# Performance work log

Measured on AMD Instinct MI355X. Metric: run time of the kernel, lower is better.

## Reference

```python
import jax, jax.numpy as jnp
import numpy as np

K = 1024      # num_embeddings
D = 256       # embedding_dim
BETA = 0.25


def setup_inputs() -> dict:
    key = jax.random.key(0)
    k1, k2 = jax.random.split(key)
    z = jax.random.normal(k1, (4, D, 16, 32, 32), dtype=jnp.float32)
    # matches torch init: uniform(-1/K, 1/K)
    embedding = jax.random.uniform(k2, (K, D), dtype=jnp.float32,
                                   minval=-1.0 / K, maxval=1.0 / K)
    return {"z": z, "embedding": embedding}


def reference(z, embedding):
    # z: (B, C, Dd, H, W) with C == D
    z_perm = jnp.transpose(z, (0, 2, 3, 4, 1))          # (B, Dd, H, W, C)
    flat = z_perm.reshape(-1, D)                        # (N, D)

    dist = (jnp.sum(flat * flat, axis=1, keepdims=True)
            + jnp.sum(embedding * embedding, axis=1)
            - 2.0 * flat @ embedding.T)
    indices_flat = jnp.argmin(dist, axis=1)             # (N,)

    # one-hot @ embedding == direct gather
    z_q_flat = embedding[indices_flat]                  # (N, D)
    z_q = z_q_flat.reshape(z_perm.shape)

    commitment_loss = jnp.mean((z_perm - jax.lax.stop_gradient(z_q)) ** 2)
    vq_loss = BETA * commitment_loss

    # straight-through estimator
    z_q_st = z_perm + jax.lax.stop_gradient(z_q - z_perm)
    z_q_out = jnp.transpose(z_q_st, (0, 4, 1, 2, 3))    # back to (B, C, Dd, H, W)

    # perplexity from assignment histogram
    n = flat.shape[0]
    counts = jnp.zeros((K,), dtype=flat.dtype).at[indices_flat].add(1.0)
    avg_probs = counts / n
    perplexity = jnp.exp(-jnp.sum(avg_probs * jnp.log(avg_probs + 1e-10)))

    indices = indices_flat.reshape(z_perm.shape[:-1])   # (B, Dd, H, W)
    return z_q_out, vq_loss, indices, perplexity
```

## Files before the change

kernel.cpp:

```cpp
#include <hip/hip_runtime.h>

#define Dd 256
#define Kc 1024
#define SPATIAL 16384
#define NROWS 65536
#define NELEM 16777216
#define LOSS_OFF 16777216
#define IDX_OFF  16777217
#define PERP_OFF (16777217 + 65536)
#define MARGIN 3.5e-4f

typedef _Float16 f16x8 __attribute__((ext_vector_type(8)));
typedef _Float16 f16x2 __attribute__((ext_vector_type(2)));
typedef float f32x4 __attribute__((ext_vector_type(4)));


__global__ __launch_bounds__(256) void prep2_kernel(const float* __restrict__ emb,
                                                    _Float16* __restrict__ ef,
                                                    float* __restrict__ se) {
  const int j = blockIdx.x, c = threadIdx.x;
  float v = emb[j * Dd + c];
  ef[j * Dd + c] = (_Float16)(v * 1024.0f);
  double s = (double)v * (double)v;
  #pragma unroll
  for (int off = 32; off; off >>= 1) s += __shfl_down(s, off, 64);
  __shared__ double ws4[4];
  if ((threadIdx.x & 63) == 0) ws4[threadIdx.x >> 6] = s;
  __syncthreads();
  if (threadIdx.x == 0) se[j] = (float)(ws4[0] + ws4[1] + ws4[2] + ws4[3]);
}

__global__ __launch_bounds__(256, 2) void prefilter2_kernel(const float* __restrict__ z,
                                                            const _Float16* __restrict__ ef,
                                                            const float* __restrict__ se,
                                                            float* __restrict__ sx,
                                                            float* __restrict__ rowmin,
                                                            int* __restrict__ candcount,
                                                            int* __restrict__ cand_g) {
  __shared__ _Float16 As[32 * 272];
  __shared__ double sxp[8][32];
  __shared__ float selds[Kc];
  __shared__ int cnts[32];
  __shared__ int cands[32][8];
  __shared__ float rminw[4][32];
  __shared__ float rthr[32];

  const int tid = threadIdx.x;
  const int n0 = blockIdx.x * 32;
  const int b = n0 >> 14, s0 = n0 & 16383;
  const float* zb = z + (size_t)b * (Dd * SPATIAL) + s0;

  {
    const int r = tid & 31, cp = tid >> 5;
    double acc = 0.0;
    #pragma unroll 8
    for (int c = cp * 32; c < cp * 32 + 32; ++c) {
      const float v = zb[(size_t)c * SPATIAL + r];
      As[r * 272 + c] = (_Float16)v;
      acc += (double)v * (double)v;
    }
    sxp[cp][r] = acc;
  }
  #pragma unroll
  for (int i = 0; i < 4; ++i) selds[tid + 256 * i] = se[tid + 256 * i];
  if (tid < 32) cnts[tid] = 0;
  __syncthreads();
  if (tid < 32) {
    double s = 0.0;
    #pragma unroll
    for (int p = 0; p < 8; ++p) s += sxp[p][tid];
    sx[n0 + tid] = (float)s;
  }

  const int w = tid >> 6, lane = tid & 63, q = lane >> 4, l15 = lane & 15;
  const int colbase = w * 256;

  f16x8 Afrag[2][8];
  #pragma unroll
  for (int rt = 0; rt < 2; ++rt)
    #pragma unroll
    for (int kk = 0; kk < 8; ++kk)
      Afrag[rt][kk] = *(const f16x8*)(&As[(rt * 16 + l15) * 272 + kk * 32 + q * 8]);

  const _Float16* efb = ef + (size_t)(colbase + l15) * Dd + q * 8;

  float rmin8[8];
  #pragma unroll
  for (int i = 0; i < 8; ++i) rmin8[i] = 3.4e38f;
  f16x2 scst[16][4];

  #pragma unroll
  for (int ct = 0; ct < 16; ++ct) {
    const _Float16* bp = efb + (size_t)ct * 16 * Dd;
    f16x8 B[8];
    #pragma unroll
    for (int kk = 0; kk < 8; ++kk) B[kk] = *(const f16x8*)(bp + kk * 32);
    f32x4 a0 = {0.f, 0.f, 0.f, 0.f}, a1 = {0.f, 0.f, 0.f, 0.f};
    #pragma unroll
    for (int kk = 0; kk < 8; ++kk) {
      a0 = __builtin_amdgcn_mfma_f32_16x16x32_f16(Afrag[0][kk], B[kk], a0, 0, 0, 0);
      a1 = __builtin_amdgcn_mfma_f32_16x16x32_f16(Afrag[1][kk], B[kk], a1, 0, 0, 0);
    }
    const float sec = selds[colbase + ct * 16 + l15];
    #pragma unroll
    for (int reg = 0; reg < 4; ++reg) {
      const float sc0 = fmaf(-0.001953125f, a0[reg], sec);
      const float sc1 = fmaf(-0.001953125f, a1[reg], sec);
      rmin8[reg]     = fminf(rmin8[reg], sc0);
      rmin8[reg + 4] = fminf(rmin8[reg + 4], sc1);
      scst[ct][reg] = (f16x2){(_Float16)sc0, (_Float16)sc1};
    }
  }

  #pragma unroll
  for (int m = 1; m <= 8; m <<= 1)
    #pragma unroll
    for (int i = 0; i < 8; ++i) rmin8[i] = fminf(rmin8[i], __shfl_xor(rmin8[i], m, 64));
  if (l15 == 0) {
    #pragma unroll
    for (int reg = 0; reg < 4; ++reg) {
      rminw[w][q * 4 + reg] = rmin8[reg];
      rminw[w][16 + q * 4 + reg] = rmin8[4 + reg];
    }
  }
  __syncthreads();
  if (tid < 32) {
    const float m = fminf(fminf(rminw[0][tid], rminw[1][tid]),
                          fminf(rminw[2][tid], rminw[3][tid]));
    rowmin[n0 + tid] = m;
    rthr[tid] = m + MARGIN;
  }
  __syncthreads();

  float thr0[4], thr1[4];
  #pragma unroll
  for (int reg = 0; reg < 4; ++reg) {
    thr0[reg] = rthr[q * 4 + reg];
    thr1[reg] = rthr[16 + q * 4 + reg];
  }
  #pragma unroll
  for (int ct = 0; ct < 16; ++ct) {
    const int col = colbase + ct * 16 + l15;
    #pragma unroll
    for (int reg = 0; reg < 4; ++reg) {
      if ((float)scst[ct][reg][0] < thr0[reg]) {
        const int pos = atomicAdd(&cnts[q * 4 + reg], 1);
        if (pos < 8) cands[q * 4 + reg][pos] = col;
      }
      if ((float)scst[ct][reg][1] < thr1[reg]) {
        const int pos = atomicAdd(&cnts[16 + q * 4 + reg], 1);
        if (pos < 8) cands[16 + q * 4 + reg][pos] = col;
      }
    }
  }
  __syncthreads();
  if (tid < 32) candcount[n0 + tid] = cnts[tid];
  cand_g[(size_t)(n0 + (tid >> 3)) * 8 + (tid & 7)] = cands[tid >> 3][tid & 7];
}

__global__ __launch_bounds__(256) void resolve_easy_kernel(const int* __restrict__ candcount,
                                                           const int* __restrict__ cand_g,
                                                           const float* __restrict__ sx,
                                                           const float* __restrict__ rowmin,
                                                           float* __restrict__ out_idx_f,
                                                           int* __restrict__ idx_i,
                                                           int* __restrict__ counts,
                                                           int* __restrict__ hardcnt,
                                                           int* __restrict__ hardlist,
                                                           double* __restrict__ loss_sum) {
  const int tid = threadIdx.x;
  const int n = blockIdx.x * 256 + tid;
  const int cnt = candcount[n];
  double lp = 0.0;
  if (cnt == 1) {
    const int j = cand_g[(size_t)n * 8];
    idx_i[n] = j;
    out_idx_f[n] = (float)j;
    atomicAdd(&counts[j], 1);
    lp = (double)sx[n] + (double)rowmin[n];
  } else {
    const int pos = atomicAdd(hardcnt, 1);
    hardlist[pos] = n;
  }
  #pragma unroll
  for (int off = 32; off; off >>= 1) lp += __shfl_down(lp, off, 64);
  __shared__ double dred[4];
  if ((tid & 63) == 0) dred[tid >> 6] = lp;
  __syncthreads();
  if (tid == 0) atomicAdd(loss_sum, dred[0] + dred[1] + dred[2] + dred[3]);
}

__global__ __launch_bounds__(256) void resolve_hard_kernel(const float* __restrict__ z,
                                                           const float* __restrict__ emb,
                                                           const float* __restrict__ se,
                                                           const float* __restrict__ sx,
                                                           const int* __restrict__ candcount,
                                                           const int* __restrict__ cand_g,
                                                           const int* __restrict__ hardcnt,
                                                           const int* __restrict__ hardlist,
                                                           float* __restrict__ out_idx_f,
                                                           int* __restrict__ idx_i,
                                                           int* __restrict__ counts,
                                                           double* __restrict__ loss_sum) {
  __shared__ float xs[4][256];
  const int tid = threadIdx.x, w = tid >> 6, lane = tid & 63;
  const int hc = *hardcnt;
  const int nw = gridDim.x * 4;
  double wloss = 0.0;
  for (int i = blockIdx.x * 4 + w; i < hc; i += nw) {
    const int n = hardlist[i];
    const int b = n >> 14, s = n & 16383;
    #pragma unroll
    for (int ro = 0; ro < 4; ++ro)
      xs[w][ro * 64 + lane] =
          z[(size_t)b * (Dd * SPATIAL) + (size_t)(ro * 64 + lane) * SPATIAL + s];
    asm volatile("s_waitcnt lgkmcnt(0) vmcnt(0)" ::: "memory");
    const int cnt = candcount[n];
    const float sxn = sx[n];
    float scb = 3.4e38f;
    int jb = 0x7fffffff;
    if (cnt <= 8) {
      if (lane < cnt) {
        jb = cand_g[(size_t)n * 8 + lane];
        const float4* ep = (const float4*)(emb + (size_t)jb * Dd);
        float acc = 0.f;
        #pragma unroll 8
        for (int kk = 0; kk < 64; ++kk) {
          const float4 e4 = ep[kk];
          const float* xp = &xs[w][kk * 4];
          acc = fmaf(xp[0], e4.x, acc);
          acc = fmaf(xp[1], e4.y, acc);
          acc = fmaf(xp[2], e4.z, acc);
          acc = fmaf(xp[3], e4.w, acc);
        }
        const float t1 = sxn + se[jb];
        scb = t1 - 2.0f * acc;
      }
    } else {
      for (int jj = 0; jj < 16; ++jj) {
        const int j = lane * 16 + jj;
        const float4* ep = (const float4*)(emb + (size_t)j * Dd);
        float acc = 0.f;
        #pragma unroll 8
        for (int kk = 0; kk < 64; ++kk) {
          const float4 e4 = ep[kk];
          const float* xp = &xs[w][kk * 4];
          acc = fmaf(xp[0], e4.x, acc);
          acc = fmaf(xp[1], e4.y, acc);
          acc = fmaf(xp[2], e4.z, acc);
          acc = fmaf(xp[3], e4.w, acc);
        }
        const float t1 = sxn + se[j];
        const float sc = t1 - 2.0f * acc;
        if (sc < scb) { scb = sc; jb = j; }
      }
    }
    #pragma unroll
    for (int m = 1; m <= 32; m <<= 1) {
      const float so = __shfl_xor(scb, m, 64);
      const int jo = __shfl_xor(jb, m, 64);
      if (so < scb || (so == scb && jo < jb)) { scb = so; jb = jo; }
    }
    if (lane == 0) {
      idx_i[n] = jb;
      out_idx_f[n] = (float)jb;
      atomicAdd(&counts[jb], 1);
      wloss += (double)sxn + (double)scb;
    }
  }
  if (lane == 0) atomicAdd(loss_sum, wloss);
}

__global__ __launch_bounds__(256) void phase2c_kernel(const float* __restrict__ emb,
                                                      const int* __restrict__ idx_i,
                                                      float* __restrict__ out_zq) {
  __shared__ float els[64 * 257];
  __shared__ int sidx[64];
  const int tid = threadIdx.x;
  const int blk = blockIdx.x, b = blk >> 8, s0 = (blk & 255) << 6;
  if (tid < 64) sidx[tid] = idx_i[b * SPATIAL + s0 + tid];
  __syncthreads();
  {
    const int rr = tid >> 2, p = tid & 3;
    const float* ep = emb + (size_t)sidx[rr] * Dd + p * 64;
    float* dl = els + rr * 257 + p * 64;
    #pragma unroll
    for (int i = 0; i < 64; i += 4) {
      const float4 e4 = *(const float4*)(ep + i);
      dl[i] = e4.x; dl[i + 1] = e4.y; dl[i + 2] = e4.z; dl[i + 3] = e4.w;
    }
  }
  __syncthreads();
  const int s = tid & 63, coff = tid >> 6;
  const size_t zb = (size_t)b * (Dd * SPATIAL);
  #pragma unroll 4
  for (int c = coff; c < Dd; c += 4)
    out_zq[zb + (size_t)c * SPATIAL + s0 + s] = els[s * 257 + c];
}

__global__ __launch_bounds__(256) void finalize_kernel(const int* __restrict__ counts,
                                                       const double* __restrict__ loss_sum,
                                                       float* __restrict__ out) {
  const int tid = threadIdx.x;
  double local = 0.0;
  for (int k = tid; k < Kc; k += 256) {
    const double p = (double)counts[k] / (double)NROWS;
    local += p * log(p + 1e-10);
  }
  #pragma unroll
  for (int off = 32; off; off >>= 1) local += __shfl_down(local, off, 64);
  __shared__ double dred[4];
  if ((tid & 63) == 0) dred[tid >> 6] = local;
  __syncthreads();
  if (tid == 0) {
    const double H = dred[0] + dred[1] + dred[2] + dred[3];
    out[PERP_OFF] = (float)exp(-H);
    out[LOSS_OFF] = (float)(0.25 * loss_sum[0] / (double)NELEM);
  }
}


__global__ __launch_bounds__(256) void prep_kernel(const float* __restrict__ emb,
                                                   float* __restrict__ eT,
                                                   float* __restrict__ se) {
  const int j = blockIdx.x, c = threadIdx.x;
  float v = emb[j * Dd + c];
  eT[c * Kc + j] = v;
  double s = (double)v * (double)v;
  #pragma unroll
  for (int off = 32; off; off >>= 1) s += __shfl_down(s, off, 64);
  __shared__ double ws4[4];
  if ((threadIdx.x & 63) == 0) ws4[threadIdx.x >> 6] = s;
  __syncthreads();
  if (threadIdx.x == 0) se[j] = (float)(ws4[0] + ws4[1] + ws4[2] + ws4[3]);
}

__global__ __launch_bounds__(256) void sx_kernel(const float* __restrict__ z,
                                                 float* __restrict__ sx) {
  __shared__ double part[4][64];
  const int tid = threadIdx.x, r = tid & 63, cg = tid >> 6;
  const int blk = blockIdx.x, b = blk >> 8, s0 = (blk & 255) << 6;
  const float* zb = z + (size_t)b * (Dd * SPATIAL);
  double acc = 0.0;
  for (int c = cg * 64; c < cg * 64 + 64; ++c) {
    const float v = zb[(size_t)c * SPATIAL + s0 + r];
    acc += (double)v * (double)v;
  }
  part[cg][r] = acc;
  __syncthreads();
  if (tid < 64)
    sx[b * SPATIAL + s0 + tid] =
        (float)(part[0][tid] + part[1][tid] + part[2][tid] + part[3][tid]);
}

__global__ __launch_bounds__(256) void argmin_kernel(const float* __restrict__ z,
                                                     const float* __restrict__ eT,
                                                     const float* __restrict__ se,
                                                     const float* __restrict__ sx,
                                                     float* __restrict__ out_idx_f,
                                                     int* __restrict__ idx_i,
                                                     int* __restrict__ counts) {
  __shared__ float As[32 * 64];
  __shared__ float Bs[32 * 64];
  __shared__ float ses[Kc];
  __shared__ float sxs[64];
  __shared__ float redS1[64 * 16];
  __shared__ int   redI1[64 * 16];
  const int tid = threadIdx.x, tc = tid & 15, tr = tid >> 4;
  const int blk = blockIdx.x, b = blk >> 8, s0 = (blk & 255) << 6;
  const float* zb = z + (size_t)b * (Dd * SPATIAL);
  #pragma unroll
  for (int i = 0; i < 4; ++i) ses[tid + 256 * i] = se[tid + 256 * i];
  if (tid < 64) sxs[tid] = sx[b * SPATIAL + s0 + tid];
  float s1[4]; int j1[4];
  #pragma unroll
  for (int r = 0; r < 4; ++r) { s1[r] = 3.4e38f; j1[r] = 0; }
  for (int j0 = 0; j0 < Kc; j0 += 64) {
    float acc[4][4];
    #pragma unroll
    for (int rr = 0; rr < 4; ++rr)
      #pragma unroll
      for (int cc = 0; cc < 4; ++cc) acc[rr][cc] = 0.0f;
    for (int c0 = 0; c0 < Dd; c0 += 32) {
      __syncthreads();
      #pragma unroll
      for (int i = 0; i < 8; ++i) {
        const int e = i * 256 + tid, ci = e >> 6, r = e & 63;
        As[e] = zb[(size_t)(c0 + ci) * SPATIAL + s0 + r];
        Bs[e] = eT[(c0 + ci) * Kc + j0 + r];
      }
      __syncthreads();
      #pragma unroll
      for (int d = 0; d < 32; ++d) {
        const float4 av = *reinterpret_cast<const float4*>(&As[d * 64 + 4 * tr]);
        const float4 bv = *reinterpret_cast<const float4*>(&Bs[d * 64 + 4 * tc]);
        const float aa[4] = {av.x, av.y, av.z, av.w};
        const float bb[4] = {bv.x, bv.y, bv.z, bv.w};
        #pragma unroll
        for (int rr = 0; rr < 4; ++rr)
          #pragma unroll
          for (int cc = 0; cc < 4; ++cc)
            acc[rr][cc] = fmaf(aa[rr], bb[cc], acc[rr][cc]);
      }
    }
    #pragma unroll
    for (int rr = 0; rr < 4; ++rr) {
      const float sxr = sxs[4 * tr + rr];
      #pragma unroll
      for (int cc = 0; cc < 4; ++cc) {
        const int j = j0 + 4 * tc + cc;
        const float t1 = sxr + ses[j];
        const float s = t1 - 2.0f * acc[rr][cc];
        if (s < s1[rr] || (s == s1[rr] && j < j1[rr])) { s1[rr] = s; j1[rr] = j; }
      }
    }
  }
  #pragma unroll
  for (int rr = 0; rr < 4; ++rr) {
    redS1[(4 * tr + rr) * 16 + tc] = s1[rr];
    redI1[(4 * tr + rr) * 16 + tc] = j1[rr];
  }
  __syncthreads();
  if (tid < 64) {
    float bs = redS1[tid * 16];
    int bj = redI1[tid * 16];
    #pragma unroll
    for (int t = 1; t < 16; ++t) {
      const float a1 = redS1[tid * 16 + t];
      const int aj = redI1[tid * 16 + t];
      if (a1 < bs || (a1 == bs && aj < bj)) { bs = a1; bj = aj; }
    }
    const int n = b * SPATIAL + s0 + tid;
    out_idx_f[n] = (float)bj;
    idx_i[n] = bj;
    atomicAdd(&counts[bj], 1);
  }
}

__global__ __launch_bounds__(256) void phase2_kernel(const float* __restrict__ z,
                                                     const float* __restrict__ eT,
                                                     const int* __restrict__ idx_i,
                                                     float* __restrict__ out_zq,
                                                     double* __restrict__ loss_sum) {
  __shared__ int sidx[64];
  __shared__ double dred[4];
  const int tid = threadIdx.x;
  const int blk = blockIdx.x, b = blk >> 8, s0 = (blk & 255) << 6;
  if (tid < 64) sidx[tid] = idx_i[b * SPATIAL + s0 + tid];
  __syncthreads();
  const int s = tid & 63, coff = tid >> 6;
  const size_t zb = (size_t)b * (Dd * SPATIAL);
  const int myidx = sidx[s];
  double lsum = 0.0;
  for (int c = coff; c < Dd; c += 4) {
    const size_t off = zb + (size_t)c * SPATIAL + s0 + s;
    const float zv = z[off];
    const float zq = eT[c * Kc + myidx];
    out_zq[off] = zv + (zq - zv);
    const float d = zv - zq;
    lsum += (double)d * (double)d;
  }
  #pragma unroll
  for (int off = 32; off; off >>= 1) lsum += __shfl_down(lsum, off, 64);
  if ((tid & 63) == 0) dred[tid >> 6] = lsum;
  __syncthreads();
  if (tid == 0) atomicAdd(loss_sum, dred[0] + dred[1] + dred[2] + dred[3]);
}


extern "C" void kernel_launch(void* const* d_in, const int* in_sizes, int n_in,
                              void* d_out, int out_size, void* d_ws, size_t ws_size,
                              hipStream_t stream) {
  const float* z   = (const float*)d_in[0];
  const float* emb = (const float*)d_in[1];
  float* out = (float*)d_out;
  char* ws = (char*)d_ws;

  const size_t OFF_SE   = 8192;
  const size_t OFF_SX   = 12288;
  const size_t OFF_EF   = 274432;
  const size_t OFF_RM   = 798720;
  const size_t OFF_IDX  = 1060864;
  const size_t OFF_CCT  = 1323008;
  const size_t OFF_CAND = 1585152;
  const size_t OFF_HARD = 3682304;
  const size_t NEED     = 3944448;

  double* loss_sum = (double*)(ws + 0);
  int*    hardcnt  = (int*)(ws + 8);
  int*    counts   = (int*)(ws + 256);

  hipMemsetAsync(d_ws, 0, 8192, stream);

  if (ws_size >= NEED) {
    float*    se        = (float*)(ws + OFF_SE);
    float*    sx        = (float*)(ws + OFF_SX);
    _Float16* ef        = (_Float16*)(ws + OFF_EF);
    float*    rowmin    = (float*)(ws + OFF_RM);
    int*      idx_i     = (int*)(ws + OFF_IDX);
    int*      candcount = (int*)(ws + OFF_CCT);
    int*      cand_g    = (int*)(ws + OFF_CAND);
    int*      hardlist  = (int*)(ws + OFF_HARD);

    prep2_kernel<<<Kc, 256, 0, stream>>>(emb, ef, se);
    prefilter2_kernel<<<2048, 256, 0, stream>>>(z, ef, se, sx, rowmin,
                                                candcount, cand_g);
    resolve_easy_kernel<<<256, 256, 0, stream>>>(candcount, cand_g, sx, rowmin,
                                                 out + IDX_OFF, idx_i, counts,
                                                 hardcnt, hardlist, loss_sum);
    resolve_hard_kernel<<<256, 256, 0, stream>>>(z, emb, se, sx, candcount, cand_g,
                                                 hardcnt, hardlist, out + IDX_OFF,
                                                 idx_i, counts, loss_sum);
    phase2c_kernel<<<1024, 256, 0, stream>>>(emb, idx_i, out);
    finalize_kernel<<<1, 256, 0, stream>>>(counts, loss_sum, out);
  } else {
    float* eT    = (float*)(ws + 8192);
    float* se    = (float*)(ws + 8192 + 1048576);
    float* sx    = (float*)(ws + 8192 + 1048576 + 4096);
    int*   idx_i = (int*)(ws + 8192 + 1048576 + 4096 + 262144);

    prep_kernel<<<Kc, 256, 0, stream>>>(emb, eT, se);
    sx_kernel<<<1024, 256, 0, stream>>>(z, sx);
    argmin_kernel<<<1024, 256, 0, stream>>>(z, eT, se, sx, out + IDX_OFF, idx_i, counts);
    phase2_kernel<<<1024, 256, 0, stream>>>(z, eT, idx_i, out, loss_sum);
    finalize_kernel<<<1, 256, 0, stream>>>(counts, loss_sum, out);
  }
}
```

Measured before the change: 327.1 us.

## Pre-swizzle codebook into MFMA fragment layout, widen prefilter blocks, vectorize z_q stores

The fp16 codebook is written in a layout that matches the MFMA B-fragment order, so each lane loads its fragment with fully coalesced contiguous 16-byte reads. The prefilter kernel moves to 512 threads with 8 waves, each covering 128 codebook columns instead of 256. This halves the per-wave score storage and register pressure and allows higher occupancy. The z_q output kernel now writes float4 vectors along the spatial axis instead of scalar stores. Risks are more LDS-reduction overhead and extra strided shared-memory reads in the output transpose.

```diff
diff --git a/kernel.cpp b/kernel.cpp
--- a/kernel.cpp
+++ b/kernel.cpp
@@ -16,11 +16,13 @@
 
 
 __global__ __launch_bounds__(256) void prep2_kernel(const float* __restrict__ emb,
-                                                    _Float16* __restrict__ ef,
+                                                    _Float16* __restrict__ efp,
                                                     float* __restrict__ se) {
   const int j = blockIdx.x, c = threadIdx.x;
   float v = emb[j * Dd + c];
-  ef[j * Dd + c] = (_Float16)(v * 1024.0f);
+  const int ct2 = j >> 4, l15 = j & 15;
+  const int kk = c >> 5, q = (c >> 3) & 3, e = c & 7;
+  efp[((size_t)(ct2 * 8 + kk) * 64 + q * 16 + l15) * 8 + e] = (_Float16)(v * 1024.0f);
   double s = (double)v * (double)v;
   #pragma unroll
   for (int off = 32; off; off >>= 1) s += __shfl_down(s, off, 64);
@@ -30,19 +32,19 @@
   if (threadIdx.x == 0) se[j] = (float)(ws4[0] + ws4[1] + ws4[2] + ws4[3]);
 }
 
-__global__ __launch_bounds__(256, 2) void prefilter2_kernel(const float* __restrict__ z,
-                                                            const _Float16* __restrict__ ef,
+__global__ __launch_bounds__(512, 4) void prefilter2_kernel(const float* __restrict__ z,
+                                                            const _Float16* __restrict__ efp,
                                                             const float* __restrict__ se,
                                                             float* __restrict__ sx,
                                                             float* __restrict__ rowmin,
                                                             int* __restrict__ candcount,
                                                             int* __restrict__ cand_g) {
   __shared__ _Float16 As[32 * 272];
-  __shared__ double sxp[8][32];
+  __shared__ double sxp[16][32];
   __shared__ float selds[Kc];
   __shared__ int cnts[32];
   __shared__ int cands[32][8];
-  __shared__ float rminw[4][32];
+  __shared__ float rminw[8][32];
   __shared__ float rthr[32];
 
   const int tid = threadIdx.x;
@@ -53,27 +55,27 @@
   {
     const int r = tid & 31, cp = tid >> 5;
     double acc = 0.0;
-    #pragma unroll 8
-    for (int c = cp * 32; c < cp * 32 + 32; ++c) {
+    #pragma unroll
+    for (int c = cp * 16; c < cp * 16 + 16; ++c) {
       const float v = zb[(size_t)c * SPATIAL + r];
       As[r * 272 + c] = (_Float16)v;
       acc += (double)v * (double)v;
     }
     sxp[cp][r] = acc;
   }
-  #pragma unroll
-  for (int i = 0; i < 4; ++i) selds[tid + 256 * i] = se[tid + 256 * i];
+  selds[tid] = se[tid];
+  selds[tid + 512] = se[tid + 512];
   if (tid < 32) cnts[tid] = 0;
   __syncthreads();
   if (tid < 32) {
     double s = 0.0;
     #pragma unroll
-    for (int p = 0; p < 8; ++p) s += sxp[p][tid];
+    for (int p = 0; p < 16; ++p) s += sxp[p][tid];
     sx[n0 + tid] = (float)s;
   }
 
   const int w = tid >> 6, lane = tid & 63, q = lane >> 4, l15 = lane & 15;
-  const int colbase = w * 256;
+  const int colbase = w * 128;
 
   f16x8 Afrag[2][8];
   #pragma unroll
@@ -82,24 +84,20 @@
     for (int kk = 0; kk < 8; ++kk)
       Afrag[rt][kk] = *(const f16x8*)(&As[(rt * 16 + l15) * 272 + kk * 32 + q * 8]);
 
-  const _Float16* efb = ef + (size_t)(colbase + l15) * Dd + q * 8;
-
   float rmin8[8];
   #pragma unroll
   for (int i = 0; i < 8; ++i) rmin8[i] = 3.4e38f;
-  f16x2 scst[16][4];
-
-  #pragma unroll
-  for (int ct = 0; ct < 16; ++ct) {
-    const _Float16* bp = efb + (size_t)ct * 16 * Dd;
-    f16x8 B[8];
-    #pragma unroll
-    for (int kk = 0; kk < 8; ++kk) B[kk] = *(const f16x8*)(bp + kk * 32);
+  f16x2 scst[8][4];
+
+  #pragma unroll
+  for (int ct = 0; ct < 8; ++ct) {
+    const _Float16* bp = efp + ((size_t)((w * 8 + ct) * 8) * 64 + lane) * 8;
     f32x4 a0 = {0.f, 0.f, 0.f, 0.f}, a1 = {0.f, 0.f, 0.f, 0.f};
     #pragma unroll
     for (int kk = 0; kk < 8; ++kk) {
-      a0 = __builtin_amdgcn_mfma_f32_16x16x32_f16(Afrag[0][kk], B[kk], a0, 0, 0, 0);
-      a1 = __builtin_amdgcn_mfma_f32_16x16x32_f16(Afrag[1][kk], B[kk], a1, 0, 0, 0);
+      const f16x8 B = *(const f16x8*)(bp + kk * 512);
+      a0 = __builtin_amdgcn_mfma_f32_16x16x32_f16(Afrag[0][kk], B, a0, 0, 0, 0);
+      a1 = __builtin_amdgcn_mfma_f32_16x16x32_f16(Afrag[1][kk], B, a1, 0, 0, 0);
     }
     const float sec = selds[colbase + ct * 16 + l15];
     #pragma unroll
@@ -125,8 +123,9 @@
   }
   __syncthreads();
   if (tid < 32) {
-    const float m = fminf(fminf(rminw[0][tid], rminw[1][tid]),
-                          fminf(rminw[2][tid], rminw[3][tid]));
+    float m = rminw[0][tid];
+    #pragma unroll
+    for (int ww = 1; ww < 8; ++ww) m = fminf(m, rminw[ww][tid]);
     rowmin[n0 + tid] = m;
     rthr[tid] = m + MARGIN;
   }
@@ -139,7 +138,7 @@
     thr1[reg] = rthr[16 + q * 4 + reg];
   }
   #pragma unroll
-  for (int ct = 0; ct < 16; ++ct) {
+  for (int ct = 0; ct < 8; ++ct) {
     const int col = colbase + ct * 16 + l15;
     #pragma unroll
     for (int reg = 0; reg < 4; ++reg) {
@@ -155,7 +154,8 @@
   }
   __syncthreads();
   if (tid < 32) candcount[n0 + tid] = cnts[tid];
-  cand_g[(size_t)(n0 + (tid >> 3)) * 8 + (tid & 7)] = cands[tid >> 3][tid & 7];
+  if (tid < 256)
+    cand_g[(size_t)(n0 + (tid >> 3)) * 8 + (tid & 7)] = cands[tid >> 3][tid & 7];
 }
 
 __global__ __launch_bounds__(256) void resolve_easy_kernel(const int* __restrict__ candcount,
@@ -291,11 +291,17 @@
     }
   }
   __syncthreads();
-  const int s = tid & 63, coff = tid >> 6;
+  const int s4 = tid & 15, cg = tid >> 4;
   const size_t zb = (size_t)b * (Dd * SPATIAL);
   #pragma unroll 4
-  for (int c = coff; c < Dd; c += 4)
-    out_zq[zb + (size_t)c * SPATIAL + s0 + s] = els[s * 257 + c];
+  for (int c = cg; c < Dd; c += 16) {
+    float4 v;
+    v.x = els[(s4 * 4 + 0) * 257 + c];
+    v.y = els[(s4 * 4 + 1) * 257 + c];
+    v.z = els[(s4 * 4 + 2) * 257 + c];
+    v.w = els[(s4 * 4 + 3) * 257 + c];
+    *(float4*)(out_zq + zb + (size_t)c * SPATIAL + s0 + s4 * 4) = v;
+  }
 }
 
 __global__ __launch_bounds__(256) void finalize_kernel(const int* __restrict__ counts,
@@ -495,15 +501,15 @@
   if (ws_size >= NEED) {
     float*    se        = (float*)(ws + OFF_SE);
     float*    sx        = (float*)(ws + OFF_SX);
-    _Float16* ef        = (_Float16*)(ws + OFF_EF);
+    _Float16* efp       = (_Float16*)(ws + OFF_EF);
     float*    rowmin    = (float*)(ws + OFF_RM);
     int*      idx_i     = (int*)(ws + OFF_IDX);
     int*      candcount = (int*)(ws + OFF_CCT);
     int*      cand_g    = (int*)(ws + OFF_CAND);
     int*      hardlist  = (int*)(ws + OFF_HARD);
 
-    prep2_kernel<<<Kc, 256, 0, stream>>>(emb, ef, se);
-    prefilter2_kernel<<<2048, 256, 0, stream>>>(z, ef, se, sx, rowmin,
+    prep2_kernel<<<Kc, 256, 0, stream>>>(emb, efp, se);
+    prefilter2_kernel<<<2048, 512, 0, stream>>>(z, efp, se, sx, rowmin,
                                                 candcount, cand_g);
     resolve_easy_kernel<<<256, 256, 0, stream>>>(candcount, cand_g, sx, rowmin,
                                                  out + IDX_OFF, idx_i, counts,
```

Result: faster. 287.9 us (-12.0%).
